# Performance work log

Measured on AMD Instinct MI355X. Metric: run time of the kernel, lower is better.

## Reference

```python
import jax, jax.numpy as jnp
import numpy as np

HID = 4096; NH = 32; NKV = 8; HD = 128; EPS = 1e-6; BASE = 10000.0

def _rmsnorm(x, w):
    # RMSNorm over last (head_dim) axis
    return x * jax.lax.rsqrt(jnp.mean(x * x, axis=-1, keepdims=True) + EPS) * w

def _rope(x, positions):
    # neox-style rotary on (b, s, h, HD): rotate halves
    half = HD // 2
    inv_freq = 1.0 / (BASE ** (jnp.arange(0, HD, 2, dtype=jnp.float32) / HD))  # (half,)
    ang = positions.astype(jnp.float32)[:, None] * inv_freq                    # (s, half)
    cos = jnp.cos(ang)[None, :, None, :]
    sin = jnp.sin(ang)[None, :, None, :]
    x1, x2 = x[..., :half], x[..., half:]
    return jnp.concatenate([x1 * cos - x2 * sin, x2 * cos + x1 * sin], axis=-1)

def setup_inputs() -> dict:
    key = jax.random.key(0)
    k0, k1, k2 = jax.random.split(key, 3)
    b, s = 4, 1024
    return {
        "h_shard": jax.random.normal(k0, (b, s, HID), jnp.float32),
        "positions": jnp.arange(s, dtype=jnp.int32),
        "w_qkv": jax.random.normal(k1, (NH * HD + 2 * NKV * HD, HID), jnp.float32) * 0.02,
        "w_o": jax.random.normal(k2, (HID, NH * HD), jnp.float32) * 0.02,
        "q_norm_w": jnp.ones((HD,), jnp.float32),
        "k_norm_w": jnp.ones((HD,), jnp.float32),
    }

def reference(h_shard, positions, w_qkv, w_o, q_norm_w, k_norm_w):
    b, s, _ = h_shard.shape
    q_sz, kv_sz = NH * HD, NKV * HD
    # fused QKV projection (world_size=1 -> ag_mm is a plain matmul x @ W.T)
    qkv = h_shard @ w_qkv.T                                   # (b, s, q_sz + 2*kv_sz)
    q = qkv[..., :q_sz].reshape(b, s, NH, HD)
    k = qkv[..., q_sz:q_sz + kv_sz].reshape(b, s, NKV, HD)
    v = qkv[..., q_sz + kv_sz:].reshape(b, s, NKV, HD)
    # per-head RMSNorm then RoPE on q/k (Qwen3 ordering)
    q = _rope(_rmsnorm(q, q_norm_w), positions)
    k = _rope(_rmsnorm(k, k_norm_w), positions)
    # GQA SDPA without materializing repeated KV: group query heads per kv head
    g = NH // NKV
    qg = q.reshape(b, s, NKV, g, HD)
    scores = jnp.einsum('bskgd,btkd->bkgst', qg, k) / jnp.sqrt(jnp.float32(HD))
    causal = jnp.tril(jnp.ones((s, s), dtype=bool))
    scores = jnp.where(causal, scores, -jnp.inf)
    probs = jax.nn.softmax(scores, axis=-1)
    attn = jnp.einsum('bkgst,btkd->bskgd', probs, v).reshape(b, s, q_sz)
    # output projection (mm_rs -> plain matmul for world_size=1)
    return attn @ w_o.T
```

## Files before the change

kernel.cpp:

```cpp
#include <hip/hip_runtime.h>

typedef __bf16 bf16;
typedef __bf16 bf16x4 __attribute__((ext_vector_type(4)));
typedef __bf16 bf16x8 __attribute__((ext_vector_type(8)));
typedef float f32x4 __attribute__((ext_vector_type(4)));

#define HID 4096
#define QKV_N 6144
#define NTOK 4096

__device__ __forceinline__ void gload_lds16(const bf16* g, bf16* l) {
  __builtin_amdgcn_global_load_lds(
      (__attribute__((address_space(1))) void*)(g),
      (__attribute__((address_space(3))) void*)(l), 16, 0, 0);
}

__global__ void cvt_kernel(const float4* __restrict__ s, bf16x4* __restrict__ d) {
  int i = blockIdx.x * blockDim.x + threadIdx.x;
  float4 v = s[i];
  bf16x4 o;
  o[0] = (bf16)v.x; o[1] = (bf16)v.y; o[2] = (bf16)v.z; o[3] = (bf16)v.w;
  d[i] = o;
}

template <typename OutT>
__global__ __launch_bounds__(256) void gemm_bt(
    const bf16* __restrict__ A, const bf16* __restrict__ Bm,
    OutT* __restrict__ C, int M, int N, int K)
{
  __shared__ bf16 As[128 * 64];
  __shared__ bf16 Bs[128 * 64];
  const int tid = threadIdx.x;
  const int w = tid >> 6, l = tid & 63;
  const int quad = l >> 4, lane16 = l & 15;
  const int row0 = blockIdx.y * 128, col0 = blockIdx.x * 128;
  const int wm = (w & 1) * 64, wn = (w >> 1) * 64;
  const int lrow = l >> 3;
  const int lkswz = ((l & 7) ^ lrow) * 8;
  const int sw = lane16 & 7;

  f32x4 acc[4][4];
#pragma unroll
  for (int a = 0; a < 4; ++a)
#pragma unroll
    for (int b = 0; b < 4; ++b) acc[a][b] = (f32x4){0.f, 0.f, 0.f, 0.f};

  for (int k0 = 0; k0 < K; k0 += 64) {
#pragma unroll
    for (int r = 0; r < 4; ++r) {
      int i = r * 4 + w;
      gload_lds16(A + (size_t)(row0 + i * 8 + lrow) * K + k0 + lkswz, &As[i * 512 + l * 8]);
      gload_lds16(Bm + (size_t)(col0 + i * 8 + lrow) * K + k0 + lkswz, &Bs[i * 512 + l * 8]);
    }
    __syncthreads();
#pragma unroll
    for (int kk = 0; kk < 2; ++kk) {
      bf16x8 af[4], bfr[4];
#pragma unroll
      for (int im = 0; im < 4; ++im)
        af[im] = *(const bf16x8*)&As[(wm + im * 16 + lane16) * 64 + (((kk * 4 + quad) ^ sw) * 8)];
#pragma unroll
      for (int in_ = 0; in_ < 4; ++in_)
        bfr[in_] = *(const bf16x8*)&Bs[(wn + in_ * 16 + lane16) * 64 + (((kk * 4 + quad) ^ sw) * 8)];
#pragma unroll
      for (int im = 0; im < 4; ++im)
#pragma unroll
        for (int in_ = 0; in_ < 4; ++in_)
          acc[im][in_] = __builtin_amdgcn_mfma_f32_16x16x32_bf16(af[im], bfr[in_], acc[im][in_], 0, 0, 0);
    }
    __syncthreads();
  }
#pragma unroll
  for (int im = 0; im < 4; ++im) {
#pragma unroll
    for (int r = 0; r < 4; ++r) {
      int row = row0 + wm + im * 16 + quad * 4 + r;
      OutT* cp = C + (size_t)row * N + col0 + wn;
#pragma unroll
      for (int in_ = 0; in_ < 4; ++in_)
        cp[in_ * 16 + lane16] = (OutT)acc[im][in_][r];
    }
  }
}

__global__ __launch_bounds__(256) void norm_rope_kernel(
    bf16* __restrict__ qkv, const int* __restrict__ pos,
    const float* __restrict__ qw, const float* __restrict__ kw)
{
  int g = blockIdx.x * 4 + (threadIdx.x >> 6);
  int tok = g / 40;
  int slot = g % 40;
  int d = threadIdx.x & 63;
  bf16* base;
  const float* w;
  if (slot < 32) { base = qkv + (size_t)tok * QKV_N + slot * 128; w = qw; }
  else           { base = qkv + (size_t)tok * QKV_N + HID + (slot - 32) * 128; w = kw; }
  float x1 = (float)base[d], x2 = (float)base[d + 64];
  float ss = x1 * x1 + x2 * x2;
#pragma unroll
  for (int m = 1; m < 64; m <<= 1) ss += __shfl_xor(ss, m, 64);
  float rn = rsqrtf(ss * (1.0f / 128.0f) + 1e-6f);
  x1 = x1 * rn * w[d];
  x2 = x2 * rn * w[d + 64];
  int p = pos[tok & 1023];
  float invf = exp2f(-0.20762050593045952f * (float)d);
  float ang = (float)p * invf;
  float sn, c;
  sincosf(ang, &sn, &c);
  base[d]      = (bf16)(x1 * c - x2 * sn);
  base[d + 64] = (bf16)(x2 * c + x1 * sn);
}

__global__ __launch_bounds__(256) void flash_kernel(
    const bf16* __restrict__ qkv, bf16* __restrict__ attn)
{
  __shared__ bf16 Ks[2][64 * 128];
  __shared__ bf16 Vt[2][128 * 64];
  __shared__ bf16 Ps[4][16 * 72];

  const int bh = blockIdx.y;
  const int qt = ((bh >> 4) & 1) ? (15 - blockIdx.x) : blockIdx.x;
  const int batch = bh >> 5;
  const int qh = bh & 31;
  const int kvh = qh >> 2;
  const int tid = threadIdx.x;
  const int w = tid >> 6, l = tid & 63;
  const int quad = l >> 4, lane16 = l & 15;
  const int sw = lane16 & 7;
  const size_t tok0 = (size_t)batch * 1024;
  const int q0 = qt * 64;

  bf16x8 qf[4];
  {
    const bf16* qrow = qkv + (tok0 + q0 + w * 16 + lane16) * QKV_N + qh * 128 + quad * 8;
#pragma unroll
    for (int kk = 0; kk < 4; ++kk) qf[kk] = *(const bf16x8*)(qrow + kk * 32);
  }

  f32x4 O[8];
#pragma unroll
  for (int id = 0; id < 8; ++id) O[id] = (f32x4){0.f, 0.f, 0.f, 0.f};
  float m_run[4], l_run[4];
#pragma unroll
  for (int r = 0; r < 4; ++r) { m_run[r] = -1e30f; l_run[r] = 0.f; }

  const float scale = 0.08838834764831845f;
  bf16x8 vreg[4];

  auto stage_K = [&](int j, int buf) {
#pragma unroll
    for (int r = 0; r < 4; ++r) {
      int i = r * 4 + w;
      int rloc = i * 4 + (l >> 4);
      int o = (l & 15) ^ (rloc & 7);
      const bf16* g = qkv + (tok0 + j * 64 + rloc) * QKV_N + HID + kvh * 128 + o * 8;
      gload_lds16(g, &Ks[buf][i * 512 + l * 8]);
    }
  };
  auto load_V = [&](int j) {
#pragma unroll
    for (int c = 0; c < 4; ++c) {
      int d0 = (c * 4 + w) * 8;
      vreg[c] = *(const bf16x8*)(qkv + (tok0 + j * 64 + l) * QKV_N + HID + 1024 + kvh * 128 + d0);
    }
  };
  auto write_V = [&](int buf) {
#pragma unroll
    for (int c = 0; c < 4; ++c) {
      int d0 = (c * 4 + w) * 8;
#pragma unroll
      for (int e = 0; e < 8; ++e) {
        int d = d0 + e;
        Vt[buf][d * 64 + (((l >> 3) ^ (d & 7)) * 8) + (l & 7)] = vreg[c][e];
      }
    }
  };

  stage_K(0, 0);
  load_V(0);
  write_V(0);
  __syncthreads();

  for (int j = 0; j <= qt; ++j) {
    const int p = j & 1;
    if (j < qt) { stage_K(j + 1, p ^ 1); load_V(j + 1); }

    f32x4 s[4];
#pragma unroll
    for (int in_ = 0; in_ < 4; ++in_) s[in_] = (f32x4){0.f, 0.f, 0.f, 0.f};
#pragma unroll
    for (int kk = 0; kk < 4; ++kk) {
#pragma unroll
      for (int in_ = 0; in_ < 4; ++in_) {
        bf16x8 b = *(const bf16x8*)&Ks[p][(in_ * 16 + lane16) * 128 + (((kk * 4 + quad) ^ sw) * 8)];
        s[in_] = __builtin_amdgcn_mfma_f32_16x16x32_bf16(qf[kk], b, s[in_], 0, 0, 0);
      }
    }

    if (j < qt) write_V(p ^ 1);

    const bool edge = (j == qt);
#pragma unroll
    for (int r = 0; r < 4; ++r) {
      float rm = -1e30f;
#pragma unroll
      for (int in_ = 0; in_ < 4; ++in_) {
        float v = s[in_][r] * scale;
        if (edge) {
          int t_abs = j * 64 + in_ * 16 + lane16;
          int q_abs = q0 + w * 16 + quad * 4 + r;
          v = (t_abs <= q_abs) ? v : -1e30f;
        }
        s[in_][r] = v;
        rm = fmaxf(rm, v);
      }
#pragma unroll
      for (int m = 1; m < 16; m <<= 1) rm = fmaxf(rm, __shfl_xor(rm, m, 64));
      float mn = fmaxf(m_run[r], rm);
      float alpha = __expf(m_run[r] - mn);
      m_run[r] = mn;
      float rs = 0.f;
#pragma unroll
      for (int in_ = 0; in_ < 4; ++in_) {
        float pv = __expf(s[in_][r] - mn);
        s[in_][r] = pv;
        rs += pv;
      }
#pragma unroll
      for (int m = 1; m < 16; m <<= 1) rs += __shfl_xor(rs, m, 64);
      l_run[r] = l_run[r] * alpha + rs;
#pragma unroll
      for (int id = 0; id < 8; ++id) O[id][r] *= alpha;
#pragma unroll
      for (int in_ = 0; in_ < 4; ++in_)
        Ps[w][(quad * 4 + r) * 72 + in_ * 16 + lane16] = (bf16)s[in_][r];
    }

#pragma unroll
    for (int kt = 0; kt < 2; ++kt) {
      bf16x8 a = *(const bf16x8*)&Ps[w][lane16 * 72 + kt * 32 + quad * 8];
#pragma unroll
      for (int id = 0; id < 8; ++id) {
        bf16x8 b = *(const bf16x8*)&Vt[p][(id * 16 + lane16) * 64 + (((kt * 4 + quad) ^ sw) * 8)];
        O[id] = __builtin_amdgcn_mfma_f32_16x16x32_bf16(a, b, O[id], 0, 0, 0);
      }
    }
    __syncthreads();
  }

#pragma unroll
  for (int r = 0; r < 4; ++r) {
    float inv = 1.0f / l_run[r];
    int row = q0 + w * 16 + quad * 4 + r;
    bf16* orow = attn + (tok0 + row) * (size_t)HID + qh * 128;
#pragma unroll
    for (int id = 0; id < 8; ++id) orow[id * 16 + lane16] = (bf16)(O[id][r] * inv);
  }
}

extern "C" void kernel_launch(void* const* d_in, const int* in_sizes, int n_in,
                              void* d_out, int out_size, void* d_ws, size_t ws_size,
                              hipStream_t stream) {
  const float* h    = (const float*)d_in[0];
  const int*   pos  = (const int*)d_in[1];
  const float* wqkv = (const float*)d_in[2];
  const float* wo   = (const float*)d_in[3];
  const float* qw   = (const float*)d_in[4];
  const float* kw   = (const float*)d_in[5];
  float* out = (float*)d_out;

  bf16* hb    = (bf16*)d_ws;
  bf16* wqkvb = hb + 16777216;
  bf16* wob   = wqkvb + 25165824;
  bf16* qkvb  = wob + 16777216;
  bf16* attnb = qkvb + 25165824;

  cvt_kernel<<<16384, 256, 0, stream>>>((const float4*)h, (bf16x4*)hb);
  cvt_kernel<<<24576, 256, 0, stream>>>((const float4*)wqkv, (bf16x4*)wqkvb);
  cvt_kernel<<<16384, 256, 0, stream>>>((const float4*)wo, (bf16x4*)wob);

  gemm_bt<bf16><<<dim3(48, 32), 256, 0, stream>>>(hb, wqkvb, qkvb, NTOK, QKV_N, HID);

  norm_rope_kernel<<<NTOK * 40 / 4, 256, 0, stream>>>(qkvb, pos, qw, kw);

  flash_kernel<<<dim3(16, 128), 256, 0, stream>>>(qkvb, attnb);

  gemm_bt<float><<<dim3(32, 32), 256, 0, stream>>>(attnb, wob, out, NTOK, HID, HID);
}
```

Baseline: 800.6 us.

## Rewrite GEMM as 256x256 double-buffered ping-pong kernel with block swizzle

Replaces the 128x128 single-buffered GEMM with a 256x256-tile, 512-thread kernel. It double-buffers LDS, issues global-to-LDS loads for later k-tiles while MFMAs run on the current one, and splits each k-step into four quadrant phases with barriers, setprio and explicit waitcnt. Block IDs are remapped in groups of 8 to improve L2 locality. The aim is to hide load latency and raise data reuse per tile, at the cost of 128KB of LDS per block, fewer blocks (384/256) on the device, and a fragile manual schedule.

```diff
diff --git a/kernel.cpp b/kernel.cpp
--- a/kernel.cpp
+++ b/kernel.cpp
@@ -24,63 +24,155 @@
 }
 
 template <typename OutT>
-__global__ __launch_bounds__(256) void gemm_bt(
+__global__ __launch_bounds__(512, 2) void gemm_bt256(
     const bf16* __restrict__ A, const bf16* __restrict__ Bm,
     OutT* __restrict__ C, int M, int N, int K)
 {
-  __shared__ bf16 As[128 * 64];
-  __shared__ bf16 Bs[128 * 64];
+  __shared__ __align__(16) bf16 As[2][256 * 64];
+  __shared__ __align__(16) bf16 Bs[2][256 * 64];
+
   const int tid = threadIdx.x;
   const int w = tid >> 6, l = tid & 63;
   const int quad = l >> 4, lane16 = l & 15;
-  const int row0 = blockIdx.y * 128, col0 = blockIdx.x * 128;
-  const int wm = (w & 1) * 64, wn = (w >> 1) * 64;
+  const int sw = lane16 & 7;
   const int lrow = l >> 3;
-  const int lkswz = ((l & 7) ^ lrow) * 8;
-  const int sw = lane16 & 7;
-
-  f32x4 acc[4][4];
-#pragma unroll
-  for (int a = 0; a < 4; ++a)
-#pragma unroll
-    for (int b = 0; b < 4; ++b) acc[a][b] = (f32x4){0.f, 0.f, 0.f, 0.f};
-
-  for (int k0 = 0; k0 < K; k0 += 64) {
-#pragma unroll
-    for (int r = 0; r < 4; ++r) {
-      int i = r * 4 + w;
-      gload_lds16(A + (size_t)(row0 + i * 8 + lrow) * K + k0 + lkswz, &As[i * 512 + l * 8]);
-      gload_lds16(Bm + (size_t)(col0 + i * 8 + lrow) * K + k0 + lkswz, &Bs[i * 512 + l * 8]);
-    }
-    __syncthreads();
-#pragma unroll
-    for (int kk = 0; kk < 2; ++kk) {
-      bf16x8 af[4], bfr[4];
+  const int lk = (l & 7) ^ lrow;
+
+  const int nwg = gridDim.x * gridDim.y;
+  int bid = blockIdx.y * gridDim.x + blockIdx.x;
+  bid = (bid & 7) * (nwg >> 3) + (bid >> 3);
+  const int row0 = (bid / gridDim.x) * 256;
+  const int col0 = (bid % gridDim.x) * 256;
+
+  const int wm = (w >> 2) * 128;
+  const int wn = (w & 3) * 64;
+
+  f32x4 acc[2][2][4][2];
+#pragma unroll
+  for (int mq = 0; mq < 2; ++mq)
+#pragma unroll
+    for (int nq = 0; nq < 2; ++nq)
 #pragma unroll
       for (int im = 0; im < 4; ++im)
-        af[im] = *(const bf16x8*)&As[(wm + im * 16 + lane16) * 64 + (((kk * 4 + quad) ^ sw) * 8)];
-#pragma unroll
-      for (int in_ = 0; in_ < 4; ++in_)
-        bfr[in_] = *(const bf16x8*)&Bs[(wn + in_ * 16 + lane16) * 64 + (((kk * 4 + quad) ^ sw) * 8)];
-#pragma unroll
-      for (int im = 0; im < 4; ++im)
-#pragma unroll
-        for (int in_ = 0; in_ < 4; ++in_)
-          acc[im][in_] = __builtin_amdgcn_mfma_f32_16x16x32_bf16(af[im], bfr[in_], acc[im][in_], 0, 0, 0);
-    }
-    __syncthreads();
+#pragma unroll
+        for (int in_ = 0; in_ < 2; ++in_) acc[mq][nq][im][in_] = (f32x4){0.f, 0.f, 0.f, 0.f};
+
+  bf16x8 af[4][2];
+  bf16x8 bf0[2][2], bf1[2][2];
+
+  auto stA = [&](int buf, int half, int kt) {
+    const bf16* g = A + (size_t)(row0 + half * 128 + w * 8 + lrow) * K + kt * 64 + lk * 8;
+    bf16* s = &As[buf][(half * 128 + w * 8) * 64 + l * 8];
+    gload_lds16(g, s);
+    gload_lds16(g + (size_t)64 * K, s + 64 * 64);
+  };
+  auto stB = [&](int buf, int half, int kt) {
+    const bf16* g = Bm + (size_t)(col0 + half * 128 + w * 8 + lrow) * K + kt * 64 + lk * 8;
+    bf16* s = &Bs[buf][(half * 128 + w * 8) * 64 + l * 8];
+    gload_lds16(g, s);
+    gload_lds16(g + (size_t)64 * K, s + 64 * 64);
+  };
+
+  auto loadA = [&](const bf16* Ap, int mq) {
+#pragma unroll
+    for (int im = 0; im < 4; ++im)
+#pragma unroll
+      for (int kk = 0; kk < 2; ++kk)
+        af[im][kk] = *(const bf16x8*)&Ap[(wm + mq * 64 + im * 16 + lane16) * 64 +
+                                         (((kk * 4 + quad) ^ sw) * 8)];
+  };
+  auto loadB = [&](const bf16* Bp, bf16x8 (&dst)[2][2], int nq) {
+#pragma unroll
+    for (int in_ = 0; in_ < 2; ++in_)
+#pragma unroll
+      for (int kk = 0; kk < 2; ++kk)
+        dst[in_][kk] = *(const bf16x8*)&Bp[(wn + nq * 32 + in_ * 16 + lane16) * 64 +
+                                           (((kk * 4 + quad) ^ sw) * 8)];
+  };
+  auto mma = [&](bf16x8 (&b)[2][2], f32x4 (&ac)[4][2]) {
+#pragma unroll
+    for (int im = 0; im < 4; ++im)
+#pragma unroll
+      for (int in_ = 0; in_ < 2; ++in_) {
+        ac[im][in_] = __builtin_amdgcn_mfma_f32_16x16x32_bf16(af[im][0], b[in_][0], ac[im][in_], 0, 0, 0);
+        ac[im][in_] = __builtin_amdgcn_mfma_f32_16x16x32_bf16(af[im][1], b[in_][1], ac[im][in_], 0, 0, 0);
+      }
+  };
+
+  const int nt = K >> 6;
+
+  stB(0, 0, 0); stB(0, 1, 0); stA(0, 0, 0); stA(0, 1, 0);
+  stB(1, 0, 1); stB(1, 1, 1); stA(1, 0, 1);
+  asm volatile("s_waitcnt vmcnt(6)" ::: "memory");
+  __builtin_amdgcn_s_barrier();
+
+  for (int t = 0; t < nt; ++t) {
+    const int p = t & 1;
+    const bf16* Ap = As[p];
+    const bf16* Bp = Bs[p];
+
+    loadA(Ap, 0);
+    loadB(Bp, bf0, 0);
+    if (t + 1 < nt) stA(p ^ 1, 1, t + 1);
+    __builtin_amdgcn_sched_barrier(0);
+    __builtin_amdgcn_s_barrier();
+    asm volatile("s_waitcnt lgkmcnt(0)" ::: "memory");
+    __builtin_amdgcn_sched_barrier(0);
+    __builtin_amdgcn_s_setprio(1);
+    mma(bf0, acc[0][0]);
+    __builtin_amdgcn_s_setprio(0);
+    __builtin_amdgcn_sched_barrier(0);
+    __builtin_amdgcn_s_barrier();
+
+    loadB(Bp, bf1, 1);
+    __builtin_amdgcn_sched_barrier(0);
+    __builtin_amdgcn_s_barrier();
+    asm volatile("s_waitcnt lgkmcnt(0)" ::: "memory");
+    __builtin_amdgcn_sched_barrier(0);
+    __builtin_amdgcn_s_setprio(1);
+    mma(bf1, acc[0][1]);
+    __builtin_amdgcn_s_setprio(0);
+    __builtin_amdgcn_sched_barrier(0);
+    __builtin_amdgcn_s_barrier();
+
+    loadA(Ap, 1);
+    if (t + 2 < nt) { stB(p, 0, t + 2); stB(p, 1, t + 2); }
+    __builtin_amdgcn_sched_barrier(0);
+    __builtin_amdgcn_s_barrier();
+    asm volatile("s_waitcnt lgkmcnt(0)" ::: "memory");
+    __builtin_amdgcn_sched_barrier(0);
+    __builtin_amdgcn_s_setprio(1);
+    mma(bf1, acc[1][1]);
+    __builtin_amdgcn_s_setprio(0);
+    __builtin_amdgcn_sched_barrier(0);
+    __builtin_amdgcn_s_barrier();
+
+    if (t + 2 < nt) stA(p, 0, t + 2);
+    __builtin_amdgcn_sched_barrier(0);
+    __builtin_amdgcn_s_barrier();
+    __builtin_amdgcn_s_setprio(1);
+    mma(bf0, acc[1][0]);
+    __builtin_amdgcn_s_setprio(0);
+    __builtin_amdgcn_sched_barrier(0);
+    if (t + 2 < nt) asm volatile("s_waitcnt vmcnt(6)" ::: "memory");
+    else            asm volatile("s_waitcnt vmcnt(0)" ::: "memory");
+    __builtin_amdgcn_s_barrier();
   }
-#pragma unroll
-  for (int im = 0; im < 4; ++im) {
-#pragma unroll
-    for (int r = 0; r < 4; ++r) {
-      int row = row0 + wm + im * 16 + quad * 4 + r;
-      OutT* cp = C + (size_t)row * N + col0 + wn;
-#pragma unroll
-      for (int in_ = 0; in_ < 4; ++in_)
-        cp[in_ * 16 + lane16] = (OutT)acc[im][in_][r];
-    }
-  }
+
+#pragma unroll
+  for (int mq = 0; mq < 2; ++mq)
+#pragma unroll
+    for (int im = 0; im < 4; ++im)
+#pragma unroll
+      for (int r = 0; r < 4; ++r) {
+        int row = row0 + wm + mq * 64 + im * 16 + quad * 4 + r;
+        OutT* cp = C + (size_t)row * N + col0 + wn;
+#pragma unroll
+        for (int nq = 0; nq < 2; ++nq)
+#pragma unroll
+          for (int in_ = 0; in_ < 2; ++in_)
+            cp[nq * 32 + in_ * 16 + lane16] = (OutT)acc[mq][nq][im][in_][r];
+      }
 }
 
 __global__ __launch_bounds__(256) void norm_rope_kernel(
@@ -279,11 +371,11 @@
   cvt_kernel<<<24576, 256, 0, stream>>>((const float4*)wqkv, (bf16x4*)wqkvb);
   cvt_kernel<<<16384, 256, 0, stream>>>((const float4*)wo, (bf16x4*)wob);
 
-  gemm_bt<bf16><<<dim3(48, 32), 256, 0, stream>>>(hb, wqkvb, qkvb, NTOK, QKV_N, HID);
+  gemm_bt256<bf16><<<dim3(24, 16), 512, 0, stream>>>(hb, wqkvb, qkvb, NTOK, QKV_N, HID);
 
   norm_rope_kernel<<<NTOK * 40 / 4, 256, 0, stream>>>(qkvb, pos, qw, kw);
 
   flash_kernel<<<dim3(16, 128), 256, 0, stream>>>(qkvb, attnb);
 
-  gemm_bt<float><<<dim3(32, 32), 256, 0, stream>>>(attnb, wob, out, NTOK, HID, HID);
-}
+  gemm_bt256<float><<<dim3(16, 16), 512, 0, stream>>>(attnb, wob, out, NTOK, HID, HID);
+}
```

After: 787.4 us. Within noise of the previous version (-1.6%).
